# Performance work log

Measured on AMD Instinct MI355X. Metric: run time of the kernel, lower is better.

Reference implementation:

```python
import jax, jax.numpy as jnp
import numpy as np

B, C, T, H, W = 4, 256, 8, 28, 28
IC = 128  # inter_channels = in_channels // 2


def setup_inputs() -> dict:
    key = jax.random.key(0)
    ks = jax.random.split(key, 5)
    s_in = 1.0 / np.sqrt(C)
    s_ic = 1.0 / np.sqrt(IC)
    return {
        "x": jax.random.normal(ks[0], (B, C, T, H, W), dtype=jnp.float32),
        "Wg": jax.random.normal(ks[1], (IC, C), dtype=jnp.float32) * s_in,
        "Wtheta": jax.random.normal(ks[2], (IC, C), dtype=jnp.float32) * s_in,
        "Wphi": jax.random.normal(ks[3], (IC, C), dtype=jnp.float32) * s_in,
        "Wz": jax.random.normal(ks[4], (C, IC), dtype=jnp.float32) * s_ic,
    }


def reference(x, Wg, Wtheta, Wphi, Wz):
    b, c, t, h, w = x.shape
    n = t * h * w
    xf = x.reshape(b, c, n)  # 1x1x1 conv == channel GEMM over flattened positions
    g_x = jnp.einsum("oc,bcn->bon", Wg, xf)       # [B, IC, N]
    theta_x = jnp.einsum("oc,bcn->bon", Wtheta, xf)
    phi_x = jnp.einsum("oc,bcn->bon", Wphi, xf)
    # f = theta^T @ phi : [B, N, N]
    f = jnp.einsum("bcn,bcm->bnm", theta_x, phi_x)
    f_div_C = jax.nn.softmax(f, axis=-1)
    # y = f_div_C @ g^T : [B, N, IC] -> keep as [B, IC, N]
    y = jnp.einsum("bnm,bcm->bcn", f_div_C, g_x)  # [B, IC, N]
    z = jnp.einsum("oc,bcn->bon", Wz, y).reshape(b, c, t, h, w) + x
    return z
```

## Files before the change

### kernel.cpp

```cpp
#include <hip/hip_runtime.h>
#include <cstdint>


#define BB   4
#define CCH  256
#define NPOS 6272
#define ICH  128
#define BNIC ((size_t)BB * NPOS * ICH)
#define KSPL 4
#define KLEN (NPOS / KSPL)
#define TKF  32
#define NITK (KLEN / TKF)
#define SLACK 12.0f

typedef __attribute__((ext_vector_type(8)))  _Float16 h8v;
typedef __attribute__((ext_vector_type(16))) float fx16;

__device__ __forceinline__ unsigned short f2h(float f) {
  _Float16 h = (_Float16)f;
  return __builtin_bit_cast(unsigned short, h);
}
__device__ __forceinline__ unsigned int pkh(float lo, float hi) {
  return __builtin_bit_cast(unsigned int, __builtin_amdgcn_cvt_pkrtz(lo, hi));
}
__device__ __forceinline__ float h2f(unsigned short u) {
  return (float)__builtin_bit_cast(_Float16, u);
}

__global__ __launch_bounds__(256, 1)
void wconv(const float* __restrict__ Wtheta, const float* __restrict__ Wphi,
           const float* __restrict__ Wg,
           unsigned short* __restrict__ Whi, unsigned short* __restrict__ Wlo) {
  const int idx4 = (blockIdx.x * 256 + threadIdx.x) * 4;
  const int p = idx4 >> 15;
  const float* W = (p == 0) ? Wtheta : (p == 1) ? Wphi : Wg;
  const float4 v = *(const float4*)&W[idx4 - (p << 15)];
  const float vv[4] = {v.x, v.y, v.z, v.w};
  ushort4 h, l;
  unsigned short* hp = (unsigned short*)&h;
  unsigned short* lp = (unsigned short*)&l;
  #pragma unroll
  for (int q = 0; q < 4; ++q) {
    _Float16 hh = (_Float16)vv[q];
    hp[q] = __builtin_bit_cast(unsigned short, hh);
    lp[q] = f2h(vv[q] - (float)hh);
  }
  *(ushort4*)&Whi[idx4] = h;
  *(ushort4*)&Wlo[idx4] = l;
}

__global__ __launch_bounds__(256, 2)
void proj_mfma(const float* __restrict__ x,
               const unsigned short* __restrict__ Whi,
               const unsigned short* __restrict__ Wlo,
               unsigned short* __restrict__ Qg,
               unsigned short* __restrict__ Kg,
               unsigned short* __restrict__ Vtg) {
  __shared__ unsigned short Xhi[32][24];
  __shared__ unsigned short Xlo[32][24];
  const int n0 = blockIdx.x * 32;
  const int b  = blockIdx.y;
  const int tid = threadIdx.x;
  const int lane = tid & 63, wv = tid >> 6;
  const int ln = lane & 31, g = lane >> 5;

  fx16 acc[3];
  acc[0] = (fx16)(0.0f); acc[1] = (fx16)(0.0f); acc[2] = (fx16)(0.0f);

  const int sn = tid & 31, cp = (tid >> 5) * 2;
  const float* xp = x + ((size_t)b * CCH + cp) * NPOS + n0 + sn;

  float pv0 = xp[0];
  float pv1 = xp[NPOS];

  for (int c0 = 0; c0 < CCH; c0 += 16) {
    {
      _Float16 h0 = (_Float16)pv0, h1 = (_Float16)pv1;
      ushort2 hh, ll;
      hh.x = __builtin_bit_cast(unsigned short, h0);
      hh.y = __builtin_bit_cast(unsigned short, h1);
      ll.x = f2h(pv0 - (float)h0);
      ll.y = f2h(pv1 - (float)h1);
      *(ushort2*)&Xhi[sn][cp] = hh;
      *(ushort2*)&Xlo[sn][cp] = ll;
    }
    if (c0 + 16 < CCH) {
      pv0 = xp[(size_t)(c0 + 16) * NPOS];
      pv1 = xp[(size_t)(c0 + 17) * NPOS];
    }
    __syncthreads();
    const h8v bxh = *(const h8v*)&Xhi[ln][g * 8];
    const h8v bxl = *(const h8v*)&Xlo[ln][g * 8];
    #pragma unroll
    for (int t = 0; t < 3; ++t) {
      const int T = wv * 3 + t;
      const size_t wb = ((size_t)(T * 32 + ln)) * CCH + c0 + g * 8;
      const h8v ah = *(const h8v*)&Whi[wb];
      const h8v al = *(const h8v*)&Wlo[wb];
      acc[t] = __builtin_amdgcn_mfma_f32_32x32x16_f16(ah, bxh, acc[t], 0, 0, 0);
      acc[t] = __builtin_amdgcn_mfma_f32_32x32x16_f16(ah, bxl, acc[t], 0, 0, 0);
      acc[t] = __builtin_amdgcn_mfma_f32_32x32x16_f16(al, bxh, acc[t], 0, 0, 0);
    }
    __syncthreads();
  }

  const float LOG2E = 1.4426950408889634f;
  const int n = n0 + ln;
  #pragma unroll
  for (int t = 0; t < 3; ++t) {
    const int T = wv * 3 + t;
    const int p = T >> 2;
    const int ot = (T & 3) * 32;
    if (p < 2) {
      unsigned short* Out = (p == 0) ? Qg : Kg;
      const float scl = (p == 0) ? LOG2E : 1.0f;
      #pragma unroll
      for (int q = 0; q < 4; ++q) {
        ushort4 v;
        v.x = f2h(acc[t][4 * q + 0] * scl);
        v.y = f2h(acc[t][4 * q + 1] * scl);
        v.z = f2h(acc[t][4 * q + 2] * scl);
        v.w = f2h(acc[t][4 * q + 3] * scl);
        *(ushort4*)&Out[((size_t)b * NPOS + n) * ICH + ot + 8 * q + 4 * g] = v;
      }
    } else {
      #pragma unroll
      for (int r = 0; r < 16; ++r) {
        const int o = ot + (r & 3) + 8 * (r >> 2) + 4 * g;
        Vtg[((size_t)b * ICH + o) * NPOS + n] = f2h(acc[t][r]);
      }
    }
  }
}

__global__ __launch_bounds__(256, 2)
void flash10(const unsigned short* __restrict__ Qg,
             const unsigned short* __restrict__ Kg,
             const unsigned short* __restrict__ Vtg,
             unsigned short* __restrict__ Opart,
             float* __restrict__ Mpart,
             float* __restrict__ Lpart) {
  __shared__ unsigned short Ks[2][TKF * 128];
  __shared__ unsigned short Vs[2][128 * 36];

  const int f   = blockIdx.x;
  const int xcd = f & 7, j = f >> 3;
  const int hi  = (j >= NITK) ? 1 : 0;
  const int slab = xcd * 2 + hi;
  const int itile = j - hi * NITK;
  const int b   = slab >> 2;
  const int spl = slab & 3;
  const int n0  = itile * 128;
  const int kb  = spl * KLEN;

  const int tid = threadIdx.x;
  const int lane = tid & 63, wv = tid >> 6;
  const int qlane = lane & 31, g = lane >> 5;
  const int swz = qlane & 15;

  h8v qf[8];
  {
    const size_t qbase = ((size_t)b * NPOS + n0 + 32 * wv + qlane) * ICH;
    #pragma unroll
    for (int cs = 0; cs < 8; ++cs)
      qf[cs] = *(const h8v*)&Qg[qbase + cs * 16 + g * 8];
  }

  {
    #pragma unroll
    for (int i = 0; i < 2; ++i) {
      const int kr = (tid >> 4) + i * 16, c = tid & 15;
      const uint4 v = *(const uint4*)&Kg[((size_t)b * NPOS + kb + kr) * ICH + c * 8];
      *(uint4*)&Ks[0][kr * 128 + (c ^ (kr & 15)) * 8] = v;
      const int idx = tid * 2 + i, dr = idx >> 2, cv = idx & 3;
      const uint4 w = *(const uint4*)&Vtg[((size_t)b * ICH + dr) * NPOS + kb + cv * 8];
      *(uint2*)&Vs[0][dr * 36 + cv * 8]     = make_uint2(w.x, w.y);
      *(uint2*)&Vs[0][dr * 36 + cv * 8 + 4] = make_uint2(w.z, w.w);
    }
  }
  __syncthreads();

  float m_run = -1e30f, m_true = -1e30f, l_run = 0.0f;
  fx16 accO[4];
  #pragma unroll
  for (int mt = 0; mt < 4; ++mt) accO[mt] = (fx16)(0.0f);

  uint4 stgK[2], stgV[2];

  for (int it = 0; it < NITK; ++it) {
    const int cur = it & 1;
    const bool pre = (it + 1 < NITK);
    if (pre) {
      const int k0n = kb + (it + 1) * TKF;
      #pragma unroll
      for (int i = 0; i < 2; ++i) {
        const int kr = (tid >> 4) + i * 16;
        stgK[i] = *(const uint4*)&Kg[((size_t)b * NPOS + k0n + kr) * ICH + (tid & 15) * 8];
        const int idx = tid * 2 + i, dr = idx >> 2, cv = idx & 3;
        stgV[i] = *(const uint4*)&Vtg[((size_t)b * ICH + dr) * NPOS + k0n + cv * 8];
      }
    }

    fx16 accS = (fx16)(0.0f);
    #pragma unroll
    for (int cs = 0; cs < 8; ++cs) {
      const h8v aK = *(const h8v*)&Ks[cur][qlane * 128 + ((2 * cs + g) ^ swz) * 8];
      accS = __builtin_amdgcn_mfma_f32_32x32x16_f16(aK, qf[cs], accS, 0, 0, 0);
    }

    float a0 = fmaxf(accS[0], accS[1]),   a1 = fmaxf(accS[2], accS[3]);
    float a2 = fmaxf(accS[4], accS[5]),   a3 = fmaxf(accS[6], accS[7]);
    float a4 = fmaxf(accS[8], accS[9]),   a5 = fmaxf(accS[10], accS[11]);
    float a6 = fmaxf(accS[12], accS[13]), a7 = fmaxf(accS[14], accS[15]);
    a0 = fmaxf(a0, a1); a2 = fmaxf(a2, a3); a4 = fmaxf(a4, a5); a6 = fmaxf(a6, a7);
    float mx = fmaxf(fmaxf(a0, a2), fmaxf(a4, a6));
    mx = fmaxf(mx, __shfl_xor(mx, 32));
    m_true = fmaxf(m_true, mx);
    const bool fold = __any(mx > m_run + SLACK);
    const float mn = fold ? fmaxf(m_run, mx) : m_run;
    float lsum = 0.0f;
    unsigned int pk[4][2];
    #pragma unroll
    for (int u = 0; u < 4; ++u) {
      const float p0 = exp2f(accS[4 * u + 0] - mn);
      const float p1 = exp2f(accS[4 * u + 1] - mn);
      const float p2 = exp2f(accS[4 * u + 2] - mn);
      const float p3 = exp2f(accS[4 * u + 3] - mn);
      lsum += (p0 + p1) + (p2 + p3);
      pk[u][0] = pkh(p0, p1);
      pk[u][1] = pkh(p2, p3);
    }
    lsum += __shfl_xor(lsum, 32);
    if (fold) {
      const float alpha = exp2f(m_run - mn);
      l_run = l_run * alpha + lsum;
      m_run = mn;
      #pragma unroll
      for (int mt = 0; mt < 4; ++mt)
        #pragma unroll
        for (int r = 0; r < 16; ++r) accO[mt][r] *= alpha;
    } else {
      l_run += lsum;
    }

    #pragma unroll
    for (int s = 0; s < 2; ++s) {
      const unsigned int s0 = pk[2 * s + (g ^ 1)][0];
      const unsigned int s1 = pk[2 * s + (g ^ 1)][1];
      const unsigned int t0 = __shfl_xor(s0, 32);
      const unsigned int t1 = __shfl_xor(s1, 32);
      union { unsigned int u[4]; h8v v; } bP;
      bP.u[0] = g ? t0 : pk[2 * s][0];
      bP.u[1] = g ? t1 : pk[2 * s][1];
      bP.u[2] = g ? pk[2 * s + 1][0] : t0;
      bP.u[3] = g ? pk[2 * s + 1][1] : t1;
      #pragma unroll
      for (int mt = 0; mt < 4; ++mt) {
        const int dr = 32 * mt + qlane;
        union { unsigned int u[4]; h8v v; } aV;
        const uint2 lo = *(const uint2*)&Vs[cur][dr * 36 + (2 * s + g) * 8];
        const uint2 hi = *(const uint2*)&Vs[cur][dr * 36 + (2 * s + g) * 8 + 4];
        aV.u[0] = lo.x; aV.u[1] = lo.y; aV.u[2] = hi.x; aV.u[3] = hi.y;
        accO[mt] = __builtin_amdgcn_mfma_f32_32x32x16_f16(aV.v, bP.v, accO[mt], 0, 0, 0);
      }
    }

    if (pre) {
      const int nb = cur ^ 1;
      #pragma unroll
      for (int i = 0; i < 2; ++i) {
        const int kr = (tid >> 4) + i * 16;
        *(uint4*)&Ks[nb][kr * 128 + ((tid & 15) ^ (kr & 15)) * 8] = stgK[i];
        const int idx = tid * 2 + i, dr = idx >> 2, cv = idx & 3;
        *(uint2*)&Vs[nb][dr * 36 + cv * 8]     = make_uint2(stgV[i].x, stgV[i].y);
        *(uint2*)&Vs[nb][dr * 36 + cv * 8 + 4] = make_uint2(stgV[i].z, stgV[i].w);
      }
    }
    __syncthreads();
  }

  const float scale = exp2f(m_run - m_true);
  const int ncol = n0 + 32 * wv + qlane;
  const size_t obase = (size_t)(b * KSPL + spl) * ICH * NPOS;
  #pragma unroll
  for (int mt = 0; mt < 4; ++mt)
    #pragma unroll
    for (int r = 0; r < 16; ++r) {
      const int d = 32 * mt + (r & 3) + 8 * (r >> 2) + 4 * g;
      Opart[obase + (size_t)d * NPOS + ncol] = f2h(accO[mt][r] * scale);
    }
  if (g == 0) {
    Mpart[(size_t)(b * KSPL + spl) * NPOS + ncol] = m_true;
    Lpart[(size_t)(b * KSPL + spl) * NPOS + ncol] = l_run * scale;
  }
}

__global__ __launch_bounds__(256, 2)
void mz_kernel(const float* __restrict__ x,
               const float* __restrict__ Wz,
               const unsigned short* __restrict__ Opart,
               const float* __restrict__ Mpart,
               const float* __restrict__ Lpart,
               float* __restrict__ out) {
  __shared__ float4 wgt[128];
  __shared__ unsigned short Yh[128][24], Yl[128][24];
  __shared__ unsigned short Wzh[128][24], Wzl[128][24];

  const int n0 = blockIdx.x * 128;
  const int c0 = blockIdx.y * 128;
  const int b  = blockIdx.z;
  const int tid = threadIdx.x;
  const int lane = tid & 63, wv = tid >> 6;
  const int ln = lane & 31, g = lane >> 5;

  if (tid < 128) {
    const int n = n0 + tid;
    float m[4], l[4];
    #pragma unroll
    for (int s = 0; s < 4; ++s) {
      m[s] = Mpart[(size_t)(b * KSPL + s) * NPOS + n];
      l[s] = Lpart[(size_t)(b * KSPL + s) * NPOS + n];
    }
    const float M0 = fmaxf(fmaxf(m[0], m[1]), fmaxf(m[2], m[3]));
    float w[4], lt = 0.0f;
    #pragma unroll
    for (int s = 0; s < 4; ++s) { w[s] = exp2f(m[s] - M0); lt += w[s] * l[s]; }
    const float inv = 1.0f / lt;
    float4 o;
    o.x = w[0] * inv; o.y = w[1] * inv; o.z = w[2] * inv; o.w = w[3] * inv;
    wgt[tid] = o;
  }
  __syncthreads();

  const int np  = tid & 63;
  const int icg = tid >> 6;
  const float4 wsA4 = wgt[2 * np];
  const float4 wsB4 = wgt[2 * np + 1];
  const float wA[4] = {wsA4.x, wsA4.y, wsA4.z, wsA4.w};
  const float wB[4] = {wsB4.x, wsB4.y, wsB4.z, wsB4.w};
  const int wc = tid >> 1, wh = (tid & 1) * 8;
  const float* Wzrow = Wz + (size_t)(c0 + wc) * ICH + wh;
  const int cpair = wv >> 1, npair = wv & 1;

  fx16 acc[2][2];
  acc[0][0] = (fx16)(0.0f); acc[0][1] = (fx16)(0.0f);
  acc[1][0] = (fx16)(0.0f); acc[1][1] = (fx16)(0.0f);

  for (int k0 = 0; k0 < ICH; k0 += 16) {
    {
      const float4 w0 = *(const float4*)&Wzrow[k0];
      const float4 w1 = *(const float4*)&Wzrow[k0 + 4];
      const float wv8[8] = {w0.x, w0.y, w0.z, w0.w, w1.x, w1.y, w1.z, w1.w};
      unsigned int hu[4], lu[4];
      #pragma unroll
      for (int q = 0; q < 4; ++q) {
        _Float16 h0 = (_Float16)wv8[2 * q], h1 = (_Float16)wv8[2 * q + 1];
        hu[q] = (unsigned int)__builtin_bit_cast(unsigned short, h0) |
                ((unsigned int)__builtin_bit_cast(unsigned short, h1) << 16);
        lu[q] = (unsigned int)f2h(wv8[2 * q] - (float)h0) |
                ((unsigned int)f2h(wv8[2 * q + 1] - (float)h1) << 16);
      }
      *(uint4*)&Wzh[wc][wh] = make_uint4(hu[0], hu[1], hu[2], hu[3]);
      *(uint4*)&Wzl[wc][wh] = make_uint4(lu[0], lu[1], lu[2], lu[3]);
    }
    {
      unsigned short h0a[4], h1a[4], l0a[4], l1a[4];
      #pragma unroll
      for (int j = 0; j < 4; ++j) {
        const int ic = k0 + icg * 4 + j;
        float y0 = 0.0f, y1 = 0.0f;
        #pragma unroll
        for (int s = 0; s < 4; ++s) {
          const unsigned int u = *(const unsigned int*)
            &Opart[((size_t)(b * KSPL + s) * ICH + ic) * NPOS + n0 + 2 * np];
          y0 += wA[s] * h2f((unsigned short)(u & 0xffff));
          y1 += wB[s] * h2f((unsigned short)(u >> 16));
        }
        _Float16 hh0 = (_Float16)y0, hh1 = (_Float16)y1;
        h0a[j] = __builtin_bit_cast(unsigned short, hh0);
        h1a[j] = __builtin_bit_cast(unsigned short, hh1);
        l0a[j] = f2h(y0 - (float)hh0);
        l1a[j] = f2h(y1 - (float)hh1);
      }
      const int kc = icg * 4;
      *(uint2*)&Yh[2 * np][kc] = make_uint2(
        (unsigned)h0a[0] | ((unsigned)h0a[1] << 16),
        (unsigned)h0a[2] | ((unsigned)h0a[3] << 16));
      *(uint2*)&Yh[2 * np + 1][kc] = make_uint2(
        (unsigned)h1a[0] | ((unsigned)h1a[1] << 16),
        (unsigned)h1a[2] | ((unsigned)h1a[3] << 16));
      *(uint2*)&Yl[2 * np][kc] = make_uint2(
        (unsigned)l0a[0] | ((unsigned)l0a[1] << 16),
        (unsigned)l0a[2] | ((unsigned)l0a[3] << 16));
      *(uint2*)&Yl[2 * np + 1][kc] = make_uint2(
        (unsigned)l1a[0] | ((unsigned)l1a[1] << 16),
        (unsigned)l1a[2] | ((unsigned)l1a[3] << 16));
    }
    __syncthreads();

    h8v Ah[2], Al[2], Bh[2], Bl[2];
    #pragma unroll
    for (int ci = 0; ci < 2; ++ci) {
      const int cr = (cpair * 2 + ci) * 32 + ln;
      Ah[ci] = *(const h8v*)&Wzh[cr][g * 8];
      Al[ci] = *(const h8v*)&Wzl[cr][g * 8];
    }
    #pragma unroll
    for (int ni = 0; ni < 2; ++ni) {
      const int nr = (npair * 2 + ni) * 32 + ln;
      Bh[ni] = *(const h8v*)&Yh[nr][g * 8];
      Bl[ni] = *(const h8v*)&Yl[nr][g * 8];
    }
    #pragma unroll
    for (int ci = 0; ci < 2; ++ci)
      #pragma unroll
      for (int ni = 0; ni < 2; ++ni) {
        acc[ci][ni] = __builtin_amdgcn_mfma_f32_32x32x16_f16(Ah[ci], Bh[ni], acc[ci][ni], 0, 0, 0);
        acc[ci][ni] = __builtin_amdgcn_mfma_f32_32x32x16_f16(Ah[ci], Bl[ni], acc[ci][ni], 0, 0, 0);
        acc[ci][ni] = __builtin_amdgcn_mfma_f32_32x32x16_f16(Al[ci], Bh[ni], acc[ci][ni], 0, 0, 0);
      }
    __syncthreads();
  }

  #pragma unroll
  for (int ci = 0; ci < 2; ++ci)
    #pragma unroll
    for (int ni = 0; ni < 2; ++ni) {
      const int n = n0 + npair * 64 + ni * 32 + ln;
      #pragma unroll
      for (int r = 0; r < 16; ++r) {
        const int c = c0 + cpair * 64 + ci * 32 + (r & 3) + 8 * (r >> 2) + 4 * g;
        const size_t base = ((size_t)(b * CCH + c)) * NPOS + n;
        out[base] = acc[ci][ni][r] + x[base];
      }
    }
}

extern "C" void kernel_launch(void* const* d_in, const int* in_sizes, int n_in,
                              void* d_out, int out_size, void* d_ws, size_t ws_size,
                              hipStream_t stream) {
  const float* x      = (const float*)d_in[0];
  const float* Wg     = (const float*)d_in[1];
  const float* Wtheta = (const float*)d_in[2];
  const float* Wphi   = (const float*)d_in[3];
  const float* Wz     = (const float*)d_in[4];
  float* out = (float*)d_out;

  unsigned short* Qg    = (unsigned short*)d_ws;
  unsigned short* Kg    = Qg + BNIC;
  unsigned short* Vtg   = Kg + BNIC;
  unsigned short* Opart = Vtg + BNIC;
  float* Mpart = (float*)(Opart + (size_t)KSPL * BNIC);
  float* Lpart = Mpart + (size_t)KSPL * BB * NPOS;

  unsigned short* Whi = Opart;
  unsigned short* Wlo = Whi + 3 * 128 * 256;

  wconv<<<dim3(96), 256, 0, stream>>>(Wtheta, Wphi, Wg, Whi, Wlo);
  proj_mfma<<<dim3(NPOS / 32, BB), 256, 0, stream>>>(x, Whi, Wlo, Qg, Kg, Vtg);
  flash10 <<<dim3(BB * KSPL * NITK), 256, 0, stream>>>(Qg, Kg, Vtg, Opart, Mpart, Lpart);
  mz_kernel<<<dim3(NPOS / 128, CCH / 128, BB), 256, 0, stream>>>(x, Wz, Opart, Mpart, Lpart, out);
}
```

Baseline: 316.3 us.

## Double K-chunk per barrier in projection and flash attention loops

The projection kernel now stages 32 channels per iteration instead of 16, with a widened LDS tile. That halves the number of barrier-separated steps and issues four global loads per thread. The flash kernel processes two 32-key tiles per barrier-separated step, staging each next tile in registers while the current one computes, with a leftover tile handled after the loop. This cuts synchronisation count and deepens overlap, but doubles LDS use in the flash kernel, which may lower occupancy. NITK=49 is hardcoded as 24 pairs plus a tail.

```diff
diff --git a/kernel.cpp b/kernel.cpp
--- a/kernel.cpp
+++ b/kernel.cpp
@@ -56,8 +56,8 @@
                unsigned short* __restrict__ Qg,
                unsigned short* __restrict__ Kg,
                unsigned short* __restrict__ Vtg) {
-  __shared__ unsigned short Xhi[32][24];
-  __shared__ unsigned short Xlo[32][24];
+  __shared__ unsigned short Xhi[32][40];
+  __shared__ unsigned short Xlo[32][40];
   const int n0 = blockIdx.x * 32;
   const int b  = blockIdx.y;
   const int tid = threadIdx.x;
@@ -67,39 +67,46 @@
   fx16 acc[3];
   acc[0] = (fx16)(0.0f); acc[1] = (fx16)(0.0f); acc[2] = (fx16)(0.0f);
 
-  const int sn = tid & 31, cp = (tid >> 5) * 2;
-  const float* xp = x + ((size_t)b * CCH + cp) * NPOS + n0 + sn;
-
-  float pv0 = xp[0];
-  float pv1 = xp[NPOS];
-
-  for (int c0 = 0; c0 < CCH; c0 += 16) {
+  const int sn = tid & 31, cq = (tid >> 5) * 4;
+  const float* xp = x + ((size_t)b * CCH + cq) * NPOS + n0 + sn;
+
+  float pv[4];
+  #pragma unroll
+  for (int q = 0; q < 4; ++q) pv[q] = xp[(size_t)q * NPOS];
+
+  for (int c0 = 0; c0 < CCH; c0 += 32) {
     {
-      _Float16 h0 = (_Float16)pv0, h1 = (_Float16)pv1;
-      ushort2 hh, ll;
-      hh.x = __builtin_bit_cast(unsigned short, h0);
-      hh.y = __builtin_bit_cast(unsigned short, h1);
-      ll.x = f2h(pv0 - (float)h0);
-      ll.y = f2h(pv1 - (float)h1);
-      *(ushort2*)&Xhi[sn][cp] = hh;
-      *(ushort2*)&Xlo[sn][cp] = ll;
-    }
-    if (c0 + 16 < CCH) {
-      pv0 = xp[(size_t)(c0 + 16) * NPOS];
-      pv1 = xp[(size_t)(c0 + 17) * NPOS];
+      ushort4 h4, l4;
+      unsigned short* hp = (unsigned short*)&h4;
+      unsigned short* lp = (unsigned short*)&l4;
+      #pragma unroll
+      for (int q = 0; q < 4; ++q) {
+        _Float16 hh = (_Float16)pv[q];
+        hp[q] = __builtin_bit_cast(unsigned short, hh);
+        lp[q] = f2h(pv[q] - (float)hh);
+      }
+      *(ushort4*)&Xhi[sn][cq] = h4;
+      *(ushort4*)&Xlo[sn][cq] = l4;
+    }
+    if (c0 + 32 < CCH) {
+      #pragma unroll
+      for (int q = 0; q < 4; ++q) pv[q] = xp[(size_t)(c0 + 32 + q) * NPOS];
     }
     __syncthreads();
-    const h8v bxh = *(const h8v*)&Xhi[ln][g * 8];
-    const h8v bxl = *(const h8v*)&Xlo[ln][g * 8];
-    #pragma unroll
-    for (int t = 0; t < 3; ++t) {
-      const int T = wv * 3 + t;
-      const size_t wb = ((size_t)(T * 32 + ln)) * CCH + c0 + g * 8;
-      const h8v ah = *(const h8v*)&Whi[wb];
-      const h8v al = *(const h8v*)&Wlo[wb];
-      acc[t] = __builtin_amdgcn_mfma_f32_32x32x16_f16(ah, bxh, acc[t], 0, 0, 0);
-      acc[t] = __builtin_amdgcn_mfma_f32_32x32x16_f16(ah, bxl, acc[t], 0, 0, 0);
-      acc[t] = __builtin_amdgcn_mfma_f32_32x32x16_f16(al, bxh, acc[t], 0, 0, 0);
+    #pragma unroll
+    for (int kc = 0; kc < 2; ++kc) {
+      const h8v bxh = *(const h8v*)&Xhi[ln][kc * 16 + g * 8];
+      const h8v bxl = *(const h8v*)&Xlo[ln][kc * 16 + g * 8];
+      #pragma unroll
+      for (int t = 0; t < 3; ++t) {
+        const int T = wv * 3 + t;
+        const size_t wb = ((size_t)(T * 32 + ln)) * CCH + c0 + kc * 16 + g * 8;
+        const h8v ah = *(const h8v*)&Whi[wb];
+        const h8v al = *(const h8v*)&Wlo[wb];
+        acc[t] = __builtin_amdgcn_mfma_f32_32x32x16_f16(ah, bxh, acc[t], 0, 0, 0);
+        acc[t] = __builtin_amdgcn_mfma_f32_32x32x16_f16(ah, bxl, acc[t], 0, 0, 0);
+        acc[t] = __builtin_amdgcn_mfma_f32_32x32x16_f16(al, bxh, acc[t], 0, 0, 0);
+      }
     }
     __syncthreads();
   }
@@ -134,14 +141,14 @@
 }
 
 __global__ __launch_bounds__(256, 2)
-void flash10(const unsigned short* __restrict__ Qg,
+void flash11(const unsigned short* __restrict__ Qg,
              const unsigned short* __restrict__ Kg,
              const unsigned short* __restrict__ Vtg,
              unsigned short* __restrict__ Opart,
              float* __restrict__ Mpart,
              float* __restrict__ Lpart) {
-  __shared__ unsigned short Ks[2][TKF * 128];
-  __shared__ unsigned short Vs[2][128 * 36];
+  __shared__ unsigned short Ks[2][2 * TKF * 128];
+  __shared__ unsigned short Vs[2][2 * 128 * 36];
 
   const int f   = blockIdx.x;
   const int xcd = f & 7, j = f >> 3;
@@ -166,16 +173,21 @@
       qf[cs] = *(const h8v*)&Qg[qbase + cs * 16 + g * 8];
   }
 
-  {
+  const int kr0 = tid >> 4, kc_ = tid & 15;
+  const size_t kgbase = (size_t)b * NPOS + kb;
+  const size_t vgbase = (size_t)b * ICH * NPOS + kb;
+
+  #pragma unroll
+  for (int t = 0; t < 2; ++t) {
     #pragma unroll
     for (int i = 0; i < 2; ++i) {
-      const int kr = (tid >> 4) + i * 16, c = tid & 15;
-      const uint4 v = *(const uint4*)&Kg[((size_t)b * NPOS + kb + kr) * ICH + c * 8];
-      *(uint4*)&Ks[0][kr * 128 + (c ^ (kr & 15)) * 8] = v;
+      const int kr = kr0 + i * 16;
+      const uint4 v = *(const uint4*)&Kg[(kgbase + t * TKF + kr) * ICH + kc_ * 8];
+      *(uint4*)&Ks[0][t * 4096 + kr * 128 + (kc_ ^ (kr & 15)) * 8] = v;
       const int idx = tid * 2 + i, dr = idx >> 2, cv = idx & 3;
-      const uint4 w = *(const uint4*)&Vtg[((size_t)b * ICH + dr) * NPOS + kb + cv * 8];
-      *(uint2*)&Vs[0][dr * 36 + cv * 8]     = make_uint2(w.x, w.y);
-      *(uint2*)&Vs[0][dr * 36 + cv * 8 + 4] = make_uint2(w.z, w.w);
+      const uint4 w = *(const uint4*)&Vtg[vgbase + (size_t)dr * NPOS + t * TKF + cv * 8];
+      *(uint2*)&Vs[0][t * 4608 + dr * 36 + cv * 8]     = make_uint2(w.x, w.y);
+      *(uint2*)&Vs[0][t * 4608 + dr * 36 + cv * 8 + 4] = make_uint2(w.z, w.w);
     }
   }
   __syncthreads();
@@ -187,27 +199,13 @@
 
   uint4 stgK[2], stgV[2];
 
-  for (int it = 0; it < NITK; ++it) {
-    const int cur = it & 1;
-    const bool pre = (it + 1 < NITK);
-    if (pre) {
-      const int k0n = kb + (it + 1) * TKF;
-      #pragma unroll
-      for (int i = 0; i < 2; ++i) {
-        const int kr = (tid >> 4) + i * 16;
-        stgK[i] = *(const uint4*)&Kg[((size_t)b * NPOS + k0n + kr) * ICH + (tid & 15) * 8];
-        const int idx = tid * 2 + i, dr = idx >> 2, cv = idx & 3;
-        stgV[i] = *(const uint4*)&Vtg[((size_t)b * ICH + dr) * NPOS + k0n + cv * 8];
-      }
-    }
-
+  auto FTILE = [&](const unsigned short* ksb, const unsigned short* vsb) {
     fx16 accS = (fx16)(0.0f);
     #pragma unroll
     for (int cs = 0; cs < 8; ++cs) {
-      const h8v aK = *(const h8v*)&Ks[cur][qlane * 128 + ((2 * cs + g) ^ swz) * 8];
+      const h8v aK = *(const h8v*)&ksb[qlane * 128 + ((2 * cs + g) ^ swz) * 8];
       accS = __builtin_amdgcn_mfma_f32_32x32x16_f16(aK, qf[cs], accS, 0, 0, 0);
     }
-
     float a0 = fmaxf(accS[0], accS[1]),   a1 = fmaxf(accS[2], accS[3]);
     float a2 = fmaxf(accS[4], accS[5]),   a3 = fmaxf(accS[6], accS[7]);
     float a4 = fmaxf(accS[8], accS[9]),   a5 = fmaxf(accS[10], accS[11]);
@@ -242,7 +240,6 @@
     } else {
       l_run += lsum;
     }
-
     #pragma unroll
     for (int s = 0; s < 2; ++s) {
       const unsigned int s0 = pk[2 * s + (g ^ 1)][0];
@@ -258,26 +255,47 @@
       for (int mt = 0; mt < 4; ++mt) {
         const int dr = 32 * mt + qlane;
         union { unsigned int u[4]; h8v v; } aV;
-        const uint2 lo = *(const uint2*)&Vs[cur][dr * 36 + (2 * s + g) * 8];
-        const uint2 hi = *(const uint2*)&Vs[cur][dr * 36 + (2 * s + g) * 8 + 4];
-        aV.u[0] = lo.x; aV.u[1] = lo.y; aV.u[2] = hi.x; aV.u[3] = hi.y;
+        const uint2 lo = *(const uint2*)&vsb[dr * 36 + (2 * s + g) * 8];
+        const uint2 hi2 = *(const uint2*)&vsb[dr * 36 + (2 * s + g) * 8 + 4];
+        aV.u[0] = lo.x; aV.u[1] = lo.y; aV.u[2] = hi2.x; aV.u[3] = hi2.y;
         accO[mt] = __builtin_amdgcn_mfma_f32_32x32x16_f16(aV.v, bP.v, accO[mt], 0, 0, 0);
       }
     }
-
-    if (pre) {
-      const int nb = cur ^ 1;
-      #pragma unroll
-      for (int i = 0; i < 2; ++i) {
-        const int kr = (tid >> 4) + i * 16;
-        *(uint4*)&Ks[nb][kr * 128 + ((tid & 15) ^ (kr & 15)) * 8] = stgK[i];
-        const int idx = tid * 2 + i, dr = idx >> 2, cv = idx & 3;
-        *(uint2*)&Vs[nb][dr * 36 + cv * 8]     = make_uint2(stgV[i].x, stgV[i].y);
-        *(uint2*)&Vs[nb][dr * 36 + cv * 8 + 4] = make_uint2(stgV[i].z, stgV[i].w);
-      }
-    }
+  };
+
+  auto LOADSTG = [&](int tile) {
+    const int k0n = tile * TKF;
+    #pragma unroll
+    for (int i = 0; i < 2; ++i) {
+      const int kr = kr0 + i * 16;
+      stgK[i] = *(const uint4*)&Kg[(kgbase + k0n + kr) * ICH + kc_ * 8];
+      const int idx = tid * 2 + i, dr = idx >> 2, cv = idx & 3;
+      stgV[i] = *(const uint4*)&Vtg[vgbase + (size_t)dr * NPOS + k0n + cv * 8];
+    }
+  };
+  auto WRITESTG = [&](int buf, int slot) {
+    #pragma unroll
+    for (int i = 0; i < 2; ++i) {
+      const int kr = kr0 + i * 16;
+      *(uint4*)&Ks[buf][slot * 4096 + kr * 128 + (kc_ ^ (kr & 15)) * 8] = stgK[i];
+      const int idx = tid * 2 + i, dr = idx >> 2, cv = idx & 3;
+      *(uint2*)&Vs[buf][slot * 4608 + dr * 36 + cv * 8]     = make_uint2(stgV[i].x, stgV[i].y);
+      *(uint2*)&Vs[buf][slot * 4608 + dr * 36 + cv * 8 + 4] = make_uint2(stgV[i].z, stgV[i].w);
+    }
+  };
+
+  for (int e = 0; e < 24; ++e) {
+    const int cur = e & 1, nb = cur ^ 1;
+    LOADSTG(2 * e + 2);
+    FTILE(&Ks[cur][0], &Vs[cur][0]);
+    WRITESTG(nb, 0);
+    const bool hasB = (2 * e + 3 < NITK);
+    if (hasB) LOADSTG(2 * e + 3);
+    FTILE(&Ks[cur][4096], &Vs[cur][4608]);
+    if (hasB) WRITESTG(nb, 1);
     __syncthreads();
   }
+  FTILE(&Ks[0][0], &Vs[0][0]);
 
   const float scale = exp2f(m_run - m_true);
   const int ncol = n0 + 32 * wv + qlane;
@@ -458,6 +476,6 @@
 
   wconv<<<dim3(96), 256, 0, stream>>>(Wtheta, Wphi, Wg, Whi, Wlo);
   proj_mfma<<<dim3(NPOS / 32, BB), 256, 0, stream>>>(x, Whi, Wlo, Qg, Kg, Vtg);
-  flash10 <<<dim3(BB * KSPL * NITK), 256, 0, stream>>>(Qg, Kg, Vtg, Opart, Mpart, Lpart);
+  flash11 <<<dim3(BB * KSPL * NITK), 256, 0, stream>>>(Qg, Kg, Vtg, Opart, Mpart, Lpart);
   mz_kernel<<<dim3(NPOS / 128, CCH / 128, BB), 256, 0, stream>>>(x, Wz, Opart, Mpart, Lpart, out);
 }
```

After: 328.5 us. +3.8%, slower.

## Template flash split count, use seven key splits, widen projection channel step

Applied to the files above, without the earlier changes.

The flash-attention and merge kernels become templates over the number of key splits. When the workspace is large enough, the launch uses 7 splits instead of 4, giving 49x7x4 blocks, which should fill the GPU better and shorten each block's serial key loop. The cost is more partial outputs to write and then merge. The XCD-aware block index remapping is replaced by a plain 3D grid, which may lose L2 locality. Separately, proj_mfma now stages 32 channels per synchronization instead of 16, halving the number of barriers.

```diff
diff --git a/kernel.cpp b/kernel.cpp
--- a/kernel.cpp
+++ b/kernel.cpp
@@ -7,10 +7,7 @@
 #define NPOS 6272
 #define ICH  128
 #define BNIC ((size_t)BB * NPOS * ICH)
-#define KSPL 4
-#define KLEN (NPOS / KSPL)
 #define TKF  32
-#define NITK (KLEN / TKF)
 #define SLACK 12.0f
 
 typedef __attribute__((ext_vector_type(8)))  _Float16 h8v;
@@ -56,8 +53,8 @@
                unsigned short* __restrict__ Qg,
                unsigned short* __restrict__ Kg,
                unsigned short* __restrict__ Vtg) {
-  __shared__ unsigned short Xhi[32][24];
-  __shared__ unsigned short Xlo[32][24];
+  __shared__ unsigned short Xhi[32][40];
+  __shared__ unsigned short Xlo[32][40];
   const int n0 = blockIdx.x * 32;
   const int b  = blockIdx.y;
   const int tid = threadIdx.x;
@@ -67,39 +64,46 @@
   fx16 acc[3];
   acc[0] = (fx16)(0.0f); acc[1] = (fx16)(0.0f); acc[2] = (fx16)(0.0f);
 
-  const int sn = tid & 31, cp = (tid >> 5) * 2;
-  const float* xp = x + ((size_t)b * CCH + cp) * NPOS + n0 + sn;
-
-  float pv0 = xp[0];
-  float pv1 = xp[NPOS];
-
-  for (int c0 = 0; c0 < CCH; c0 += 16) {
+  const int sn = tid & 31, cq = (tid >> 5) * 4;
+  const float* xp = x + ((size_t)b * CCH + cq) * NPOS + n0 + sn;
+
+  float pv[4];
+  #pragma unroll
+  for (int q = 0; q < 4; ++q) pv[q] = xp[(size_t)q * NPOS];
+
+  for (int c0 = 0; c0 < CCH; c0 += 32) {
     {
-      _Float16 h0 = (_Float16)pv0, h1 = (_Float16)pv1;
-      ushort2 hh, ll;
-      hh.x = __builtin_bit_cast(unsigned short, h0);
-      hh.y = __builtin_bit_cast(unsigned short, h1);
-      ll.x = f2h(pv0 - (float)h0);
-      ll.y = f2h(pv1 - (float)h1);
-      *(ushort2*)&Xhi[sn][cp] = hh;
-      *(ushort2*)&Xlo[sn][cp] = ll;
-    }
-    if (c0 + 16 < CCH) {
-      pv0 = xp[(size_t)(c0 + 16) * NPOS];
-      pv1 = xp[(size_t)(c0 + 17) * NPOS];
+      ushort4 h4, l4;
+      unsigned short* hp = (unsigned short*)&h4;
+      unsigned short* lp = (unsigned short*)&l4;
+      #pragma unroll
+      for (int q = 0; q < 4; ++q) {
+        _Float16 hh = (_Float16)pv[q];
+        hp[q] = __builtin_bit_cast(unsigned short, hh);
+        lp[q] = f2h(pv[q] - (float)hh);
+      }
+      *(ushort4*)&Xhi[sn][cq] = h4;
+      *(ushort4*)&Xlo[sn][cq] = l4;
+    }
+    if (c0 + 32 < CCH) {
+      #pragma unroll
+      for (int q = 0; q < 4; ++q) pv[q] = xp[(size_t)(c0 + 32 + q) * NPOS];
     }
     __syncthreads();
-    const h8v bxh = *(const h8v*)&Xhi[ln][g * 8];
-    const h8v bxl = *(const h8v*)&Xlo[ln][g * 8];
-    #pragma unroll
-    for (int t = 0; t < 3; ++t) {
-      const int T = wv * 3 + t;
-      const size_t wb = ((size_t)(T * 32 + ln)) * CCH + c0 + g * 8;
-      const h8v ah = *(const h8v*)&Whi[wb];
-      const h8v al = *(const h8v*)&Wlo[wb];
-      acc[t] = __builtin_amdgcn_mfma_f32_32x32x16_f16(ah, bxh, acc[t], 0, 0, 0);
-      acc[t] = __builtin_amdgcn_mfma_f32_32x32x16_f16(ah, bxl, acc[t], 0, 0, 0);
-      acc[t] = __builtin_amdgcn_mfma_f32_32x32x16_f16(al, bxh, acc[t], 0, 0, 0);
+    #pragma unroll
+    for (int kc = 0; kc < 2; ++kc) {
+      const h8v bxh = *(const h8v*)&Xhi[ln][kc * 16 + g * 8];
+      const h8v bxl = *(const h8v*)&Xlo[ln][kc * 16 + g * 8];
+      #pragma unroll
+      for (int t = 0; t < 3; ++t) {
+        const int T = wv * 3 + t;
+        const size_t wb = ((size_t)(T * 32 + ln)) * CCH + c0 + kc * 16 + g * 8;
+        const h8v ah = *(const h8v*)&Whi[wb];
+        const h8v al = *(const h8v*)&Wlo[wb];
+        acc[t] = __builtin_amdgcn_mfma_f32_32x32x16_f16(ah, bxh, acc[t], 0, 0, 0);
+        acc[t] = __builtin_amdgcn_mfma_f32_32x32x16_f16(ah, bxl, acc[t], 0, 0, 0);
+        acc[t] = __builtin_amdgcn_mfma_f32_32x32x16_f16(al, bxh, acc[t], 0, 0, 0);
+      }
     }
     __syncthreads();
   }
@@ -133,26 +137,23 @@
   }
 }
 
+template <int KS>
 __global__ __launch_bounds__(256, 2)
-void flash10(const unsigned short* __restrict__ Qg,
+void flash_t(const unsigned short* __restrict__ Qg,
              const unsigned short* __restrict__ Kg,
              const unsigned short* __restrict__ Vtg,
              unsigned short* __restrict__ Opart,
              float* __restrict__ Mpart,
              float* __restrict__ Lpart) {
+  constexpr int KLEN = NPOS / KS;
+  constexpr int NIT  = KLEN / TKF;
   __shared__ unsigned short Ks[2][TKF * 128];
   __shared__ unsigned short Vs[2][128 * 36];
 
-  const int f   = blockIdx.x;
-  const int xcd = f & 7, j = f >> 3;
-  const int hi  = (j >= NITK) ? 1 : 0;
-  const int slab = xcd * 2 + hi;
-  const int itile = j - hi * NITK;
-  const int b   = slab >> 2;
-  const int spl = slab & 3;
-  const int n0  = itile * 128;
+  const int b   = blockIdx.z;
+  const int spl = blockIdx.y;
+  const int n0  = blockIdx.x * 128;
   const int kb  = spl * KLEN;
-
   const int tid = threadIdx.x;
   const int lane = tid & 63, wv = tid >> 6;
   const int qlane = lane & 31, g = lane >> 5;
@@ -187,9 +188,9 @@
 
   uint4 stgK[2], stgV[2];
 
-  for (int it = 0; it < NITK; ++it) {
+  for (int it = 0; it < NIT; ++it) {
     const int cur = it & 1;
-    const bool pre = (it + 1 < NITK);
+    const bool pre = (it + 1 < NIT);
     if (pre) {
       const int k0n = kb + (it + 1) * TKF;
       #pragma unroll
@@ -281,7 +282,7 @@
 
   const float scale = exp2f(m_run - m_true);
   const int ncol = n0 + 32 * wv + qlane;
-  const size_t obase = (size_t)(b * KSPL + spl) * ICH * NPOS;
+  const size_t obase = (size_t)(b * KS + spl) * ICH * NPOS;
   #pragma unroll
   for (int mt = 0; mt < 4; ++mt)
     #pragma unroll
@@ -290,19 +291,20 @@
       Opart[obase + (size_t)d * NPOS + ncol] = f2h(accO[mt][r] * scale);
     }
   if (g == 0) {
-    Mpart[(size_t)(b * KSPL + spl) * NPOS + ncol] = m_true;
-    Lpart[(size_t)(b * KSPL + spl) * NPOS + ncol] = l_run * scale;
-  }
-}
-
+    Mpart[(size_t)(b * KS + spl) * NPOS + ncol] = m_true;
+    Lpart[(size_t)(b * KS + spl) * NPOS + ncol] = l_run * scale;
+  }
+}
+
+template <int KS>
 __global__ __launch_bounds__(256, 2)
-void mz_kernel(const float* __restrict__ x,
-               const float* __restrict__ Wz,
-               const unsigned short* __restrict__ Opart,
-               const float* __restrict__ Mpart,
-               const float* __restrict__ Lpart,
-               float* __restrict__ out) {
-  __shared__ float4 wgt[128];
+void mz_t(const float* __restrict__ x,
+          const float* __restrict__ Wz,
+          const unsigned short* __restrict__ Opart,
+          const float* __restrict__ Mpart,
+          const float* __restrict__ Lpart,
+          float* __restrict__ out) {
+  __shared__ float wgt[128][8];
   __shared__ unsigned short Yh[128][24], Yl[128][24];
   __shared__ unsigned short Wzh[128][24], Wzl[128][24];
 
@@ -315,29 +317,28 @@
 
   if (tid < 128) {
     const int n = n0 + tid;
-    float m[4], l[4];
-    #pragma unroll
-    for (int s = 0; s < 4; ++s) {
-      m[s] = Mpart[(size_t)(b * KSPL + s) * NPOS + n];
-      l[s] = Lpart[(size_t)(b * KSPL + s) * NPOS + n];
-    }
-    const float M0 = fmaxf(fmaxf(m[0], m[1]), fmaxf(m[2], m[3]));
-    float w[4], lt = 0.0f;
-    #pragma unroll
-    for (int s = 0; s < 4; ++s) { w[s] = exp2f(m[s] - M0); lt += w[s] * l[s]; }
+    float m[KS], l[KS];
+    float M0 = -1e30f;
+    #pragma unroll
+    for (int s = 0; s < KS; ++s) {
+      m[s] = Mpart[(size_t)(b * KS + s) * NPOS + n];
+      l[s] = Lpart[(size_t)(b * KS + s) * NPOS + n];
+      M0 = fmaxf(M0, m[s]);
+    }
+    float w[KS], lt = 0.0f;
+    #pragma unroll
+    for (int s = 0; s < KS; ++s) { w[s] = exp2f(m[s] - M0); lt += w[s] * l[s]; }
     const float inv = 1.0f / lt;
-    float4 o;
-    o.x = w[0] * inv; o.y = w[1] * inv; o.z = w[2] * inv; o.w = w[3] * inv;
-    wgt[tid] = o;
+    #pragma unroll
+    for (int s = 0; s < KS; ++s) wgt[tid][s] = w[s] * inv;
   }
   __syncthreads();
 
   const int np  = tid & 63;
   const int icg = tid >> 6;
-  const float4 wsA4 = wgt[2 * np];
-  const float4 wsB4 = wgt[2 * np + 1];
-  const float wA[4] = {wsA4.x, wsA4.y, wsA4.z, wsA4.w};
-  const float wB[4] = {wsB4.x, wsB4.y, wsB4.z, wsB4.w};
+  float wA[KS], wB[KS];
+  #pragma unroll
+  for (int s = 0; s < KS; ++s) { wA[s] = wgt[2 * np][s]; wB[s] = wgt[2 * np + 1][s]; }
   const int wc = tid >> 1, wh = (tid & 1) * 8;
   const float* Wzrow = Wz + (size_t)(c0 + wc) * ICH + wh;
   const int cpair = wv >> 1, npair = wv & 1;
@@ -370,9 +371,9 @@
         const int ic = k0 + icg * 4 + j;
         float y0 = 0.0f, y1 = 0.0f;
         #pragma unroll
-        for (int s = 0; s < 4; ++s) {
+        for (int s = 0; s < KS; ++s) {
           const unsigned int u = *(const unsigned int*)
-            &Opart[((size_t)(b * KSPL + s) * ICH + ic) * NPOS + n0 + 2 * np];
+            &Opart[((size_t)(b * KS + s) * ICH + ic) * NPOS + n0 + 2 * np];
           y0 += wA[s] * h2f((unsigned short)(u & 0xffff));
           y1 += wB[s] * h2f((unsigned short)(u >> 16));
         }
@@ -450,14 +451,25 @@
   unsigned short* Kg    = Qg + BNIC;
   unsigned short* Vtg   = Kg + BNIC;
   unsigned short* Opart = Vtg + BNIC;
-  float* Mpart = (float*)(Opart + (size_t)KSPL * BNIC);
-  float* Lpart = Mpart + (size_t)KSPL * BB * NPOS;
 
   unsigned short* Whi = Opart;
   unsigned short* Wlo = Whi + 3 * 128 * 256;
 
   wconv<<<dim3(96), 256, 0, stream>>>(Wtheta, Wphi, Wg, Whi, Wlo);
   proj_mfma<<<dim3(NPOS / 32, BB), 256, 0, stream>>>(x, Whi, Wlo, Qg, Kg, Vtg);
-  flash10 <<<dim3(BB * KSPL * NITK), 256, 0, stream>>>(Qg, Kg, Vtg, Opart, Mpart, Lpart);
-  mz_kernel<<<dim3(NPOS / 128, CCH / 128, BB), 256, 0, stream>>>(x, Wz, Opart, Mpart, Lpart, out);
-}
+
+  const size_t need7 = (3 + 7) * BNIC * 2 + (size_t)2 * 7 * BB * NPOS * 4;
+  if (ws_size >= need7) {
+    constexpr int KS = 7;
+    float* Mpart = (float*)(Opart + (size_t)KS * BNIC);
+    float* Lpart = Mpart + (size_t)KS * BB * NPOS;
+    flash_t<KS><<<dim3(NPOS / 128, KS, BB), 256, 0, stream>>>(Qg, Kg, Vtg, Opart, Mpart, Lpart);
+    mz_t<KS><<<dim3(NPOS / 128, CCH / 128, BB), 256, 0, stream>>>(x, Wz, Opart, Mpart, Lpart, out);
+  } else {
+    constexpr int KS = 4;
+    float* Mpart = (float*)(Opart + (size_t)KS * BNIC);
+    float* Lpart = Mpart + (size_t)KS * BB * NPOS;
+    flash_t<KS><<<dim3(NPOS / 128, KS, BB), 256, 0, stream>>>(Qg, Kg, Vtg, Opart, Mpart, Lpart);
+    mz_t<KS><<<dim3(NPOS / 128, CCH / 128, BB), 256, 0, stream>>>(x, Wz, Opart, Mpart, Lpart, out);
+  }
+}
```

New measurement: 311.0 us. Within noise of the previous version (-1.7%).
